# Kernel tuning notes

Measured on AMD Instinct MI355X. Metric: run time of the kernel, lower is better.

Reference implementation:

```python
import jax, jax.numpy as jnp
import numpy as np


def setup_inputs() -> dict:
    key = jax.random.key(0)
    ks = jax.random.split(key, 11)
    B, E, R, D = 2048, 20000, 500, 256
    inp = {
        "h": jax.random.uniform(ks[0], (B, E), dtype=jnp.float32),
        "t": jax.random.uniform(ks[1], (B, E), dtype=jnp.float32),
        "r": jax.random.uniform(ks[2], (B, R), dtype=jnp.float32),
        "W_er": jax.random.normal(ks[3], (D, E), dtype=jnp.float32) * 0.02,
        "W_ei": jax.random.normal(ks[4], (D, E), dtype=jnp.float32) * 0.02,
        "W_ej": jax.random.normal(ks[5], (D, E), dtype=jnp.float32) * 0.02,
        "W_ek": jax.random.normal(ks[6], (D, E), dtype=jnp.float32) * 0.02,
        "W_rr": jax.random.normal(ks[7], (D, R), dtype=jnp.float32) * 0.02,
        "W_ri": jax.random.normal(ks[8], (D, R), dtype=jnp.float32) * 0.02,
        "W_rj": jax.random.normal(ks[9], (D, R), dtype=jnp.float32) * 0.02,
        "W_rk": jax.random.normal(ks[10], (D, R), dtype=jnp.float32) * 0.02,
    }
    return inp


def reference(h, t, r, W_er, W_ei, W_ej, W_ek, W_rr, W_ri, W_rj, W_rk):
    # entity / relation projections (nn.Linear, no bias): x @ W^T -> [B, D]
    H_r, H_i, H_j, H_k = h @ W_er.T, h @ W_ei.T, h @ W_ej.T, h @ W_ek.T
    T_r, T_i, T_j, T_k = t @ W_er.T, t @ W_ei.T, t @ W_ej.T, t @ W_ek.T
    R_r, R_i, R_j, R_k = r @ W_rr.T, r @ W_ri.T, r @ W_rj.T, r @ W_rk.T

    # hypercomplex norm per row: sqrt(|R_r|^2 + |R_i|^2 + |R_j|^2 + |R_k|^2) -> [B,1]
    norm = jnp.sqrt(
        jnp.sum(R_r * R_r + R_i * R_i + R_j * R_j + R_k * R_k, axis=1, keepdims=True)
    )
    R_r, R_i, R_j, R_k = norm * R_r, norm * R_i, norm * R_j, norm * R_k

    # Hamilton product H (x) R
    Q_r = H_r * R_r - H_i * R_i - H_j * R_j - H_k * R_k
    Q_i = H_r * R_i + H_i * R_r + H_j * R_k - H_k * R_j
    Q_j = H_r * R_j - H_i * R_k + H_j * R_r + H_k * R_i
    Q_k = H_r * R_k + H_i * R_j - H_j * R_i + H_k * R_r

    # diag(Q @ T^T) == rowwise dot sum(Q*T, axis=1) -- O(B*d) form of the anti-pattern
    score = jnp.sum(Q_r * T_r + Q_i * T_i + Q_j * T_j + Q_k * T_k, axis=1, keepdims=True)
    return jax.nn.sigmoid(score)
```

## Files before the change

### kernel.cpp

```cpp
#include <hip/hip_runtime.h>


using bf16x8 = __attribute__((ext_vector_type(8))) short;
using f32x4  = __attribute__((ext_vector_type(4))) float;
using f32x16 = __attribute__((ext_vector_type(16))) float;

#define DEVINL static __device__ __forceinline__

DEVINL void split2(float x0, float x1, unsigned& h, unsigned& l) {
  unsigned u0 = __float_as_uint(x0), u1 = __float_as_uint(x1);
  unsigned h0 = u0 & 0xFFFF0000u, h1 = u1 & 0xFFFF0000u;
  h = (u0 >> 16) | h1;
  float r0 = x0 - __uint_as_float(h0);
  float r1 = x1 - __uint_as_float(h1);
  l = (__float_as_uint(r0) >> 16) | (__float_as_uint(r1) & 0xFFFF0000u);
}

DEVINL void gload16(const void* g, void* l) {
  __builtin_amdgcn_global_load_lds(
      (const __attribute__((address_space(1))) unsigned*)g,
      (__attribute__((address_space(3))) unsigned*)l, 16, 0, 0);
}

DEVINL void conv_body(const float* srow, int srcK, int kt, int rb,
                      char* dst, int ktiles, float ld[64][36], int t)
{
  {
    int r = t >> 2, kc = (t & 3) * 8;
    int k0 = kt * 32 + kc;
    const float* s = srow + (size_t)r * srcK;
    float4 v0, v1;
    if (k0 + 8 <= srcK) {
      v0 = *(const float4*)(s + k0);
      v1 = *(const float4*)(s + k0 + 4);
    } else {
      float x[8];
#pragma unroll
      for (int j = 0; j < 8; ++j) x[j] = (k0 + j < srcK) ? s[k0 + j] : 0.f;
      v0 = make_float4(x[0], x[1], x[2], x[3]);
      v1 = make_float4(x[4], x[5], x[6], x[7]);
    }
    *(float4*)&ld[r][kc]     = v0;
    *(float4*)&ld[r][kc + 4] = v1;
  }
  __syncthreads();
  {
    int g = t >> 7, s = (t >> 6) & 1, kh = (t >> 5) & 1, r31 = t & 31;
    int row = g * 32 + r31;
    int k = s * 16 + kh * 8;
    float x[8];
#pragma unroll
    for (int j = 0; j < 8; ++j) x[j] = ld[row][k + j];
    unsigned hh[4], llv[4];
    split2(x[0], x[1], hh[0], llv[0]);
    split2(x[2], x[3], hh[1], llv[1]);
    split2(x[4], x[5], hh[2], llv[2]);
    split2(x[6], x[7], hh[3], llv[3]);
    int tile_rt = rb >> 2;
    int gbase = (rb & 3) * 2;
    char* base = dst + ((size_t)tile_rt * ktiles + kt) * 32768
               + (gbase + g) * 2048 + s * 1024 + kh * 512 + r31 * 16;
    *(uint4*)base           = make_uint4(hh[0], hh[1], hh[2], hh[3]);
    *(uint4*)(base + 16384) = make_uint4(llv[0], llv[1], llv[2], llv[3]);
  }
}

__global__ void convert_img2(const float* __restrict__ src0,
                             const float* __restrict__ src1, int rows0,
                             int srcK, char* __restrict__ dst, int ktiles)
{
  __shared__ float ld[64][36];
  const int kt = blockIdx.x, rb = blockIdx.y, t = threadIdx.x;
  int row0 = rb * 64;
  const float* srow = (row0 < rows0) ? (src0 + (size_t)row0 * srcK)
                                     : (src1 + (size_t)(row0 - rows0) * srcK);
  conv_body(srow, srcK, kt, rb, dst, ktiles, ld, t);
}

__global__ void convert_q4(const float* __restrict__ p0, const float* __restrict__ p1,
                           const float* __restrict__ p2, const float* __restrict__ p3,
                           int rbPerQ, int srcK, char* __restrict__ dst,
                           size_t qStride, int ktiles)
{
  __shared__ float ld[64][36];
  const int kt = blockIdx.x, t = threadIdx.x;
  const int q = blockIdx.y / rbPerQ, rb = blockIdx.y % rbPerQ;
  const float* src = (q == 0) ? p0 : (q == 1) ? p1 : (q == 2) ? p2 : p3;
  conv_body(src + (size_t)(rb * 64) * srcK, srcK, kt, rb,
            dst + (size_t)q * qStride, ktiles, ld, t);
}

__global__ __launch_bounds__(512, 1) void gemm_img(
    const char* __restrict__ Aimg, const char* __restrict__ Bimg, int ktiles,
    float* __restrict__ C, int MT, int NT, int KS, int swz)
{
  __shared__ __align__(16) char smem[131072];
  const int bid = blockIdx.x;

  int mt, nt, ks;
  if (swz) {
    int x = bid & 7, w = bid >> 3;
    nt = w & 3;
    int g = x + (w >> 2) * 8;
    mt = g & 15; ks = g >> 4;
  } else {
    nt = bid % NT; int q = bid / NT; mt = q % MT; ks = q / MT;
  }

  const int kt0 = (ktiles * ks) / KS;
  const int kt1 = (ktiles * (ks + 1)) / KS;

  const char* Ab = Aimg + ((size_t)mt * ktiles + kt0) * 32768;
  const char* Bb = Bimg + ((size_t)nt * ktiles + kt0) * 32768;

  const int wid = threadIdx.x >> 6, lane = threadIdx.x & 63;
  const int wr = wid >> 2, wc = wid & 3;

  f32x16 acc[4][2];
#pragma unroll
  for (int mb = 0; mb < 4; ++mb)
#pragma unroll
    for (int nb = 0; nb < 2; ++nb)
#pragma unroll
      for (int e = 0; e < 16; ++e) acc[mb][nb][e] = 0.f;

  {
    const char* As = Ab + wid * 4096 + lane * 16;
    const char* Bs = Bb + wid * 4096 + lane * 16;
#pragma unroll
    for (int i = 0; i < 4; ++i) gload16(As + i * 1024, smem + wid * 4096 + i * 1024);
#pragma unroll
    for (int i = 0; i < 4; ++i) gload16(Bs + i * 1024, smem + 32768 + wid * 4096 + i * 1024);
  }
  asm volatile("s_waitcnt vmcnt(0)" ::: "memory");
  __builtin_amdgcn_s_barrier();

  for (int kt = kt0; kt < kt1; ++kt) {
    char* bufc = smem + (size_t)((kt - kt0) & 1) * 65536;
    char* bufn = smem + (size_t)(((kt - kt0) & 1) ^ 1) * 65536;
    const bool nx = (kt + 1 < kt1);

    if (nx) {
      const char* As = Ab + (size_t)(kt + 1 - kt0) * 32768 + wid * 4096 + lane * 16;
      const char* Bs = Bb + (size_t)(kt + 1 - kt0) * 32768 + wid * 4096 + lane * 16;
#pragma unroll
      for (int i = 0; i < 4; ++i) gload16(As + i * 1024, bufn + wid * 4096 + i * 1024);
#pragma unroll
      for (int i = 0; i < 4; ++i) gload16(Bs + i * 1024, bufn + 32768 + wid * 4096 + i * 1024);
    }

    bf16x8 bh[2][2], bl[2][2];
#pragma unroll
    for (int nb = 0; nb < 2; ++nb)
#pragma unroll
      for (int s = 0; s < 2; ++s) {
        const char* p = bufc + 32768 + (wc * 2 + nb) * 2048 + s * 1024 + lane * 16;
        bh[nb][s] = *(const bf16x8*)p;
        bl[nb][s] = *(const bf16x8*)(p + 16384);
      }

    __builtin_amdgcn_s_setprio(1);
#pragma unroll
    for (int mb = 0; mb < 4; ++mb) {
      const char* p = bufc + (wr * 4 + mb) * 2048 + lane * 16;
      bf16x8 ah0 = *(const bf16x8*)(p);
      bf16x8 al0 = *(const bf16x8*)(p + 16384);
      bf16x8 ah1 = *(const bf16x8*)(p + 1024);
      bf16x8 al1 = *(const bf16x8*)(p + 1024 + 16384);
#pragma unroll
      for (int nb = 0; nb < 2; ++nb) {
        f32x16* a = &acc[mb][nb];
        *a = __builtin_amdgcn_mfma_f32_32x32x16_bf16(ah0, bh[nb][0], *a, 0, 0, 0);
        *a = __builtin_amdgcn_mfma_f32_32x32x16_bf16(al0, bh[nb][0], *a, 0, 0, 0);
        *a = __builtin_amdgcn_mfma_f32_32x32x16_bf16(ah0, bl[nb][0], *a, 0, 0, 0);
        *a = __builtin_amdgcn_mfma_f32_32x32x16_bf16(ah1, bh[nb][1], *a, 0, 0, 0);
        *a = __builtin_amdgcn_mfma_f32_32x32x16_bf16(al1, bh[nb][1], *a, 0, 0, 0);
        *a = __builtin_amdgcn_mfma_f32_32x32x16_bf16(ah1, bl[nb][1], *a, 0, 0, 0);
      }
    }
    __builtin_amdgcn_s_setprio(0);

    asm volatile("s_waitcnt vmcnt(0)" ::: "memory");
    __builtin_amdgcn_s_barrier();
  }

  float* Cb = C + (size_t)ks * (size_t)(MT * 256) * 1024;
  const long rowbase = (long)mt * 256 + wr * 128 + 4 * (lane >> 5);
  const long colbase = (long)nt * 256 + wc * 64 + (lane & 31);
#pragma unroll
  for (int mb = 0; mb < 4; ++mb)
#pragma unroll
    for (int nb = 0; nb < 2; ++nb)
#pragma unroll
      for (int reg = 0; reg < 16; ++reg) {
        long row = rowbase + mb * 32 + (reg & 3) + 8 * (reg >> 2);
        long col = colbase + nb * 32;
        Cb[(size_t)row * 1024 + col] = acc[mb][nb][reg];
      }
}

__global__ __launch_bounds__(256) void epilogue_v4(
    const float* __restrict__ C1, const float* __restrict__ C2,
    float* __restrict__ out, int KS1, int KS2)
{
  const int w = threadIdx.x >> 6, lane = threadIdx.x & 63;
  const int b = blockIdx.x * 4 + w;
  const size_t SZ1 = 4096ull * 1024ull;
  const size_t SZ2 = 2048ull * 1024ull;
  const int c4 = lane * 4;

  float H[4][4], T[4][4], R[4][4];
#pragma unroll
  for (int q = 0; q < 4; ++q) {
    float4 hv = make_float4(0.f, 0.f, 0.f, 0.f);
    float4 tv = make_float4(0.f, 0.f, 0.f, 0.f);
    float4 rv = make_float4(0.f, 0.f, 0.f, 0.f);
    for (int ks = 0; ks < KS1; ++ks) {
      float4 a = *(const float4*)(C1 + ks * SZ1 + (size_t)b * 1024 + q * 256 + c4);
      float4 c = *(const float4*)(C1 + ks * SZ1 + (size_t)(b + 2048) * 1024 + q * 256 + c4);
      hv.x += a.x; hv.y += a.y; hv.z += a.z; hv.w += a.w;
      tv.x += c.x; tv.y += c.y; tv.z += c.z; tv.w += c.w;
    }
    for (int ks = 0; ks < KS2; ++ks) {
      float4 a = *(const float4*)(C2 + ks * SZ2 + (size_t)b * 1024 + q * 256 + c4);
      rv.x += a.x; rv.y += a.y; rv.z += a.z; rv.w += a.w;
    }
    H[q][0] = hv.x; H[q][1] = hv.y; H[q][2] = hv.z; H[q][3] = hv.w;
    T[q][0] = tv.x; T[q][1] = tv.y; T[q][2] = tv.z; T[q][3] = tv.w;
    R[q][0] = rv.x; R[q][1] = rv.y; R[q][2] = rv.z; R[q][3] = rv.w;
  }

  float ss = 0.f, nn = 0.f;
#pragma unroll
  for (int j = 0; j < 4; ++j) {
    float Hr = H[0][j], Hi = H[1][j], Hj = H[2][j], Hk = H[3][j];
    float Tr = T[0][j], Ti = T[1][j], Tj = T[2][j], Tk = T[3][j];
    float Rr = R[0][j], Ri = R[1][j], Rj = R[2][j], Rk = R[3][j];
    nn += Rr*Rr + Ri*Ri + Rj*Rj + Rk*Rk;
    float Qr = Hr*Rr - Hi*Ri - Hj*Rj - Hk*Rk;
    float Qi = Hr*Ri + Hi*Rr + Hj*Rk - Hk*Rj;
    float Qj = Hr*Rj - Hi*Rk + Hj*Rr + Hk*Ri;
    float Qk = Hr*Rk + Hi*Rj - Hj*Ri + Hk*Rr;
    ss += Qr*Tr + Qi*Ti + Qj*Tj + Qk*Tk;
  }
#pragma unroll
  for (int o = 32; o; o >>= 1) {
    ss += __shfl_xor(ss, o);
    nn += __shfl_xor(nn, o);
  }
  if (lane == 0) {
    float score = sqrtf(nn) * ss;
    out[b] = 1.f / (1.f + expf(-score));
  }
}

__global__ void convert_b16(const float* __restrict__ src, int srcK,
                            char* __restrict__ dst)
{
  const int tile = blockIdx.x;
  const int wrow = threadIdx.x;
  char* base = dst + (size_t)tile * 32768;
  const float* srow = src + (size_t)wrow * srcK;
#pragma unroll
  for (int kc8 = 0; kc8 < 4; ++kc8) {
    int k0 = tile * 32 + kc8 * 8;
    float x[8];
    if (k0 + 8 <= srcK) {
      float4 v0 = *(const float4*)(srow + k0);
      float4 v1 = *(const float4*)(srow + k0 + 4);
      x[0] = v0.x; x[1] = v0.y; x[2] = v0.z; x[3] = v0.w;
      x[4] = v1.x; x[5] = v1.y; x[6] = v1.z; x[7] = v1.w;
    } else {
#pragma unroll
      for (int j = 0; j < 8; ++j) x[j] = (k0 + j < srcK) ? srow[k0 + j] : 0.f;
    }
    unsigned hh[4], ll[4];
    split2(x[0], x[1], hh[0], ll[0]);
    split2(x[2], x[3], hh[1], ll[1]);
    split2(x[4], x[5], hh[2], ll[2]);
    split2(x[6], x[7], hh[3], ll[3]);
    int lchunk = (wrow & 15) + kc8 * 16;
    int n16 = wrow >> 4;
    *(uint4*)(base + (size_t)n16 * 1024 + lchunk * 16)         = make_uint4(hh[0], hh[1], hh[2], hh[3]);
    *(uint4*)(base + 16384 + (size_t)n16 * 1024 + lchunk * 16) = make_uint4(ll[0], ll[1], ll[2], ll[3]);
  }
}

__global__ void pad_r(const float* __restrict__ src, float* __restrict__ dst)
{
  int row = blockIdx.y;
  int k = threadIdx.x * 4;
  float4 v = make_float4(0.f, 0.f, 0.f, 0.f);
  if (k + 3 < 500) v = *(const float4*)(src + (size_t)row * 500 + k);
  *(float4*)(dst + (size_t)row * 512 + k) = v;
}

__global__ __launch_bounds__(512, 2) void gemm3p(
    const float* __restrict__ A0, const float* __restrict__ A1, int mtA0, long lda,
    const char* __restrict__ Bimg, int ktilesTot,
    float* __restrict__ C, long ldc, int MT, int NT, int KS, int swz)
{
  extern __shared__ char smemd[];
  const int tid = threadIdx.x;
  const int bid = blockIdx.x;

  int mt, nt, ks;
  if (swz) {
    int x = bid & 7, w = bid >> 3;
    nt = w & 3;
    int g = x + (w >> 2) * 8;
    mt = g & 15; ks = g >> 4;
  } else {
    nt = bid % NT; int q = bid / NT; mt = q % MT; ks = q / MT;
  }

  const int kt0 = (ktilesTot * ks) / KS;
  const int kt1 = (ktilesTot * (ks + 1)) / KS;

  const float* Ablk = (mt < mtA0) ? (A0 + (size_t)mt * 256 * lda)
                                  : (A1 + (size_t)(mt - mtA0) * 256 * lda);
  const char* Bt = Bimg + ((size_t)nt * ktilesTot + kt0) * 32768;

  const int wid = tid >> 6, lane = tid & 63;
  const int wr = wid >> 2, wc = wid & 3;
  const int l15 = lane & 15, lq = lane >> 4;

  const float* aSrc = Ablk + (size_t)(wid * 32 + (lane >> 3)) * lda
                      + (size_t)kt0 * 32 + 4 * (lane & 7);

  int awoff[4];
  {
    int kg = (lane & 7) >> 1, half = lane & 1;
#pragma unroll
    for (int i = 0; i < 4; ++i) {
      int m15 = (lane >> 3) + 8 * (i & 1);
      awoff[i] = (2 * wid + (i >> 1)) * 2048 + (((m15 ^ kg) + kg * 16) << 4) + half * 8;
    }
  }
  const int aroff = (((l15 ^ lq) + lq * 16) << 4);
  const int bbase = 32768 + (wc * 4) * 1024 + lane * 16;

  f32x4 acc[8][4];
#pragma unroll
  for (int m = 0; m < 8; ++m)
#pragma unroll
    for (int j = 0; j < 4; ++j)
#pragma unroll
      for (int e = 0; e < 4; ++e) acc[m][j][e] = 0.f;

  float4 aR[4];

#define ISSUE_A(KT)                                                            \
  {                                                                            \
    const float* p_ = aSrc + (size_t)((KT) - kt0) * 32;                        \
    _Pragma("unroll")                                                          \
    for (int i = 0; i < 4; ++i) aR[i] = *(const float4*)(p_ + (size_t)(8 * i) * lda); \
  }
#define ISSUE_B(DST, KT)                                                       \
  {                                                                            \
    const char* p_ = Bt + (size_t)((KT) - kt0) * 32768 + wid * 4096 + lane * 16; \
    _Pragma("unroll")                                                          \
    for (int i = 0; i < 4; ++i)                                                \
      gload16(p_ + i * 1024, (DST) + 32768 + wid * 4096 + i * 1024);           \
  }
#define WRITE_A(DST)                                                           \
  {                                                                            \
    _Pragma("unroll")                                                          \
    for (int i = 0; i < 4; ++i) {                                              \
      unsigned h0_, l0_, h1_, l1_;                                             \
      split2(aR[i].x, aR[i].y, h0_, l0_);                                      \
      split2(aR[i].z, aR[i].w, h1_, l1_);                                      \
      *(uint2*)((DST) + awoff[i])        = make_uint2(h0_, h1_);               \
      *(uint2*)((DST) + awoff[i] + 1024) = make_uint2(l0_, l1_);               \
    }                                                                          \
  }

  ISSUE_A(kt0);
  ISSUE_B(smemd, kt0);
  WRITE_A(smemd);
  asm volatile("s_waitcnt vmcnt(0)" ::: "memory");
  asm volatile("s_waitcnt lgkmcnt(0)" ::: "memory");
  __builtin_amdgcn_s_barrier();

  for (int kt = kt0; kt < kt1; ++kt) {
    char* bufc = smemd + (size_t)((kt - kt0) & 1) * 65536;
    char* bufn = smemd + (size_t)(((kt - kt0) & 1) ^ 1) * 65536;
    const bool nx = (kt + 1 < kt1);

    if (nx) { ISSUE_A(kt + 1); ISSUE_B(bufn, kt + 1); }

    bf16x8 bh[4], bl[4];
#pragma unroll
    for (int j = 0; j < 4; ++j) {
      bh[j] = *(const bf16x8*)(bufc + bbase + j * 1024);
      bl[j] = *(const bf16x8*)(bufc + bbase + j * 1024 + 16384);
    }

    __builtin_amdgcn_s_setprio(1);
#pragma unroll
    for (int m = 0; m < 4; ++m) {
      const char* ab = bufc + (wr * 8 + m) * 2048;
      bf16x8 ah = *(const bf16x8*)(ab + aroff);
      bf16x8 al = *(const bf16x8*)(ab + aroff + 1024);
#pragma unroll
      for (int j = 0; j < 4; ++j) {
        acc[m][j] = __builtin_amdgcn_mfma_f32_16x16x32_bf16(ah, bh[j], acc[m][j], 0, 0, 0);
        acc[m][j] = __builtin_amdgcn_mfma_f32_16x16x32_bf16(al, bh[j], acc[m][j], 0, 0, 0);
        acc[m][j] = __builtin_amdgcn_mfma_f32_16x16x32_bf16(ah, bl[j], acc[m][j], 0, 0, 0);
      }
    }
    __builtin_amdgcn_s_setprio(0);

    __builtin_amdgcn_sched_barrier(0);
    if (nx) WRITE_A(bufn);

    __builtin_amdgcn_s_setprio(1);
#pragma unroll
    for (int m = 4; m < 8; ++m) {
      const char* ab = bufc + (wr * 8 + m) * 2048;
      bf16x8 ah = *(const bf16x8*)(ab + aroff);
      bf16x8 al = *(const bf16x8*)(ab + aroff + 1024);
#pragma unroll
      for (int j = 0; j < 4; ++j) {
        acc[m][j] = __builtin_amdgcn_mfma_f32_16x16x32_bf16(ah, bh[j], acc[m][j], 0, 0, 0);
        acc[m][j] = __builtin_amdgcn_mfma_f32_16x16x32_bf16(al, bh[j], acc[m][j], 0, 0, 0);
        acc[m][j] = __builtin_amdgcn_mfma_f32_16x16x32_bf16(ah, bl[j], acc[m][j], 0, 0, 0);
      }
    }
    __builtin_amdgcn_s_setprio(0);

    asm volatile("s_waitcnt vmcnt(0)" ::: "memory");
    asm volatile("s_waitcnt lgkmcnt(0)" ::: "memory");
    __builtin_amdgcn_s_barrier();
  }
#undef ISSUE_A
#undef ISSUE_B
#undef WRITE_A

  float* Cb = C + (size_t)ks * (size_t)(MT * 256) * (size_t)ldc;
  const long rowbase = (long)mt * 256 + wr * 128 + lq * 4;
  const long colbase = (long)nt * 256 + wc * 64 + l15;
#pragma unroll
  for (int m = 0; m < 8; ++m)
#pragma unroll
    for (int j = 0; j < 4; ++j)
#pragma unroll
      for (int reg = 0; reg < 4; ++reg) {
        long row = rowbase + m * 16 + reg;
        long col = colbase + j * 16;
        Cb[(size_t)row * ldc + col] = acc[m][j][reg];
      }
}

__global__ void epilogue_kernel(const float* __restrict__ C1, const float* __restrict__ C2,
                                float* __restrict__ out, int KS1, int KS2)
{
  const int b = blockIdx.x;
  const int d = threadIdx.x;
  const size_t SZ1 = 4096ull * 1024ull;
  const size_t SZ2 = 2048ull * 1024ull;

  float Hq[4], Tq[4], Rq[4];
#pragma unroll
  for (int q = 0; q < 4; ++q) {
    float hv = 0.f, tv = 0.f, rv = 0.f;
    for (int ks = 0; ks < KS1; ++ks) {
      hv += C1[ks * SZ1 + (size_t)b * 1024 + q * 256 + d];
      tv += C1[ks * SZ1 + (size_t)(b + 2048) * 1024 + q * 256 + d];
    }
    for (int ks = 0; ks < KS2; ++ks)
      rv += C2[ks * SZ2 + (size_t)b * 1024 + q * 256 + d];
    Hq[q] = hv; Tq[q] = tv; Rq[q] = rv;
  }
  float nn = Rq[0]*Rq[0] + Rq[1]*Rq[1] + Rq[2]*Rq[2] + Rq[3]*Rq[3];
  float Qr = Hq[0]*Rq[0] - Hq[1]*Rq[1] - Hq[2]*Rq[2] - Hq[3]*Rq[3];
  float Qi = Hq[0]*Rq[1] + Hq[1]*Rq[0] + Hq[2]*Rq[3] - Hq[3]*Rq[2];
  float Qj = Hq[0]*Rq[2] - Hq[1]*Rq[3] + Hq[2]*Rq[0] + Hq[3]*Rq[1];
  float Qk = Hq[0]*Rq[3] + Hq[1]*Rq[2] - Hq[2]*Rq[1] + Hq[3]*Rq[0];
  float ss = Qr*Tq[0] + Qi*Tq[1] + Qj*Tq[2] + Qk*Tq[3];

#pragma unroll
  for (int o = 32; o; o >>= 1) {
    ss += __shfl_xor(ss, o);
    nn += __shfl_xor(nn, o);
  }
  __shared__ float red[8];
  int lane = d & 63, w = d >> 6;
  if (lane == 0) { red[w] = ss; red[4 + w] = nn; }
  __syncthreads();
  if (d == 0) {
    float S = red[0] + red[1] + red[2] + red[3];
    float N = red[4] + red[5] + red[6] + red[7];
    float score = sqrtf(N) * S;
    out[b] = 1.f / (1.f + expf(-score));
  }
}

extern "C" void kernel_launch(void* const* d_in, const int* in_sizes, int n_in,
                              void* d_out, int out_size, void* d_ws, size_t ws_size,
                              hipStream_t stream)
{
  const float* h = (const float*)d_in[0];
  const float* t = (const float*)d_in[1];
  const float* r = (const float*)d_in[2];
  const float* We[4] = {(const float*)d_in[3], (const float*)d_in[4],
                        (const float*)d_in[5], (const float*)d_in[6]};
  const float* Wr[4] = {(const float*)d_in[7], (const float*)d_in[8],
                        (const float*)d_in[9], (const float*)d_in[10]};
  float* out = (float*)d_out;
  char* ws = (char*)d_ws;

  const size_t offA  = 0;
  const size_t offB  = 327680000;
  const size_t offWr = offB + 81920000;
  const size_t offRi = offWr + 2097152;
  const size_t offC1 = offRi + 4194304;
  const size_t C1sz  = 4096ull * 1024ull * 4ull;
  const size_t C2sz  = 2048ull * 1024ull * 4ull;
  const size_t needImg = offC1 + 4 * C1sz;

  if (ws_size >= needImg) {
    float* C1 = (float*)(ws + offC1);
    float* C2 = (float*)(ws + offB);
    const int KS2 = 8;

    convert_img2<<<dim3(625, 64), 256, 0, stream>>>(h, t, 2048, 20000, ws + offA, 625);
    convert_q4<<<dim3(625, 16), 256, 0, stream>>>(
        We[0], We[1], We[2], We[3], 4, 20000, ws + offB, (size_t)625 * 32768, 625);
    convert_q4<<<dim3(16, 16), 256, 0, stream>>>(
        Wr[0], Wr[1], Wr[2], Wr[3], 4, 500, ws + offWr, (size_t)16 * 32768, 16);
    convert_img2<<<dim3(16, 32), 256, 0, stream>>>(r, r, 2048, 500, ws + offRi, 16);

    gemm_img<<<dim3(256), 512, 0, stream>>>(
        ws + offA, ws + offB, 625, C1, 16, 4, 4, 1);
    gemm_img<<<dim3(8 * 4 * KS2), 512, 0, stream>>>(
        ws + offRi, ws + offWr, 16, C2, 8, 4, KS2, 0);

    epilogue_v4<<<dim3(512), 256, 0, stream>>>(C1, C2, out, 4, KS2);
    return;
  }

  const size_t fB  = 0;
  const size_t fWr = 81920000;
  const size_t fR  = fWr + 2097152;
  const size_t fC1 = fR + 4194304;
  const int KS = (ws_size >= fC1 + 4 * C1sz + 8388608ull) ? 4 : 2;
  const size_t fC2 = fC1 + (size_t)KS * C1sz;

  float* rpad = (float*)(ws + fR);
  float* C1   = (float*)(ws + fC1);
  float* C2   = (float*)(ws + fC2);

  for (int q = 0; q < 4; ++q) {
    convert_b16<<<dim3(625), 256, 0, stream>>>(We[q], 20000, ws + fB + (size_t)q * 625 * 32768);
    convert_b16<<<dim3(16), 256, 0, stream>>>(Wr[q], 500, ws + fWr + (size_t)q * 16 * 32768);
  }
  pad_r<<<dim3(1, 2048), 128, 0, stream>>>(r, rpad);

  gemm3p<<<dim3(16 * 4 * KS), 512, 131072, stream>>>(
      h, t, 8, 20000L, (const char*)(ws + fB), 625,
      C1, 1024L, 16, 4, KS, KS == 4 ? 1 : 0);
  gemm3p<<<dim3(32), 512, 131072, stream>>>(
      rpad, rpad, 8, 512L, (const char*)(ws + fWr), 16,
      C2, 1024L, 8, 4, 1, 0);

  epilogue_kernel<<<dim3(2048), 256, 0, stream>>>(C1, C2, out, KS, 1);
}
```

Baseline: 594.5 us.

## Replace double-buffered GEMM loop with four-slot half-tile ring pipeline

Splits each K tile into two half-steps and keeps a four-slot shared-memory ring, issuing loads three stages ahead. The old loop waited on all outstanding loads with vmcnt(0) every step; the new loop uses partial vmcnt waits so global-to-LDS transfers overlap with MFMA work. The cost is a more intricate prologue and epilogue sequence, with a risk of stalls or wrong results if the vmcnt counts or slot reuse are off. The MFMA count per tile and the LDS footprint of 128KB stay the same.

Measured after the change: 574.7 us. -3.3%, faster.

```diff
diff --git a/kernel.cpp b/kernel.cpp
--- a/kernel.cpp
+++ b/kernel.cpp
@@ -90,7 +90,7 @@
             dst + (size_t)q * qStride, ktiles, ld, t);
 }
 
-__global__ __launch_bounds__(512, 1) void gemm_img(
+__global__ __launch_bounds__(512, 1) void gemm_ring(
     const char* __restrict__ Aimg, const char* __restrict__ Bimg, int ktiles,
     float* __restrict__ C, int MT, int NT, int KS, int swz)
 {
@@ -109,6 +109,7 @@
 
   const int kt0 = (ktiles * ks) / KS;
   const int kt1 = (ktiles * (ks + 1)) / KS;
+  const int nsteps = 2 * (kt1 - kt0);
 
   const char* Ab = Aimg + ((size_t)mt * ktiles + kt0) * 32768;
   const char* Bb = Bimg + ((size_t)nt * ktiles + kt0) * 32768;
@@ -124,65 +125,77 @@
 #pragma unroll
       for (int e = 0; e < 16; ++e) acc[mb][nb][e] = 0.f;
 
-  {
-    const char* As = Ab + wid * 4096 + lane * 16;
-    const char* Bs = Bb + wid * 4096 + lane * 16;
-#pragma unroll
-    for (int i = 0; i < 4; ++i) gload16(As + i * 1024, smem + wid * 4096 + i * 1024);
-#pragma unroll
-    for (int i = 0; i < 4; ++i) gload16(Bs + i * 1024, smem + 32768 + wid * 4096 + i * 1024);
-  }
+#define STAGE(S)                                                               \
+  {                                                                            \
+    char* slot_ = smem + ((S) & 3) * 32768;                                    \
+    const char* At_ = Ab + (size_t)((S) >> 1) * 32768;                         \
+    const char* Bt_ = Bb + (size_t)((S) >> 1) * 32768;                         \
+    const int ko_ = ((S) & 1) * 1024;                                          \
+    _Pragma("unroll")                                                          \
+    for (int i = 0; i < 2; ++i) {                                              \
+      int p_ = 2 * wid + i;                                                    \
+      int src_ = (p_ >> 3) * 16384 + (p_ & 7) * 2048 + ko_ + lane * 16;        \
+      gload16(At_ + src_, slot_ + p_ * 1024);                                  \
+      gload16(Bt_ + src_, slot_ + 16384 + p_ * 1024);                          \
+    }                                                                          \
+  }
+#define COMPUTE(S)                                                             \
+  {                                                                            \
+    const char* slot_ = smem + ((S) & 3) * 32768;                              \
+    bf16x8 a_[4][2], b_[2][2];                                                 \
+    _Pragma("unroll")                                                          \
+    for (int mb = 0; mb < 4; ++mb)                                             \
+      _Pragma("unroll")                                                        \
+      for (int pl = 0; pl < 2; ++pl)                                           \
+        a_[mb][pl] = *(const bf16x8*)(slot_ + (pl * 8 + wr * 4 + mb) * 1024    \
+                                      + lane * 16);                            \
+    _Pragma("unroll")                                                          \
+    for (int nb = 0; nb < 2; ++nb)                                             \
+      _Pragma("unroll")                                                        \
+      for (int pl = 0; pl < 2; ++pl)                                           \
+        b_[nb][pl] = *(const bf16x8*)(slot_ + 16384                            \
+                                      + (pl * 8 + wc * 2 + nb) * 1024         \
+                                      + lane * 16);                            \
+    __builtin_amdgcn_s_setprio(1);                                             \
+    _Pragma("unroll")                                                          \
+    for (int mb = 0; mb < 4; ++mb)                                             \
+      _Pragma("unroll")                                                        \
+      for (int nb = 0; nb < 2; ++nb) {                                         \
+        f32x16* c_ = &acc[mb][nb];                                             \
+        *c_ = __builtin_amdgcn_mfma_f32_32x32x16_bf16(a_[mb][0], b_[nb][0], *c_, 0, 0, 0); \
+        *c_ = __builtin_amdgcn_mfma_f32_32x32x16_bf16(a_[mb][1], b_[nb][0], *c_, 0, 0, 0); \
+        *c_ = __builtin_amdgcn_mfma_f32_32x32x16_bf16(a_[mb][0], b_[nb][1], *c_, 0, 0, 0); \
+      }                                                                        \
+    __builtin_amdgcn_s_setprio(0);                                             \
+  }
+
+  STAGE(0); STAGE(1); STAGE(2);
+  asm volatile("s_waitcnt vmcnt(8)" ::: "memory");
+  __builtin_amdgcn_sched_barrier(0);
+  __builtin_amdgcn_s_barrier();
+
+  int s = 0;
+  for (; s + 3 < nsteps; ++s) {
+    STAGE(s + 3);
+    __builtin_amdgcn_sched_barrier(0);
+    COMPUTE(s);
+    __builtin_amdgcn_sched_barrier(0);
+    asm volatile("s_waitcnt vmcnt(8)" ::: "memory");
+    __builtin_amdgcn_s_barrier();
+  }
+  COMPUTE(s);
+  __builtin_amdgcn_sched_barrier(0);
+  asm volatile("s_waitcnt vmcnt(4)" ::: "memory");
+  __builtin_amdgcn_s_barrier();
+  ++s;
+  COMPUTE(s);
+  __builtin_amdgcn_sched_barrier(0);
   asm volatile("s_waitcnt vmcnt(0)" ::: "memory");
   __builtin_amdgcn_s_barrier();
-
-  for (int kt = kt0; kt < kt1; ++kt) {
-    char* bufc = smem + (size_t)((kt - kt0) & 1) * 65536;
-    char* bufn = smem + (size_t)(((kt - kt0) & 1) ^ 1) * 65536;
-    const bool nx = (kt + 1 < kt1);
-
-    if (nx) {
-      const char* As = Ab + (size_t)(kt + 1 - kt0) * 32768 + wid * 4096 + lane * 16;
-      const char* Bs = Bb + (size_t)(kt + 1 - kt0) * 32768 + wid * 4096 + lane * 16;
-#pragma unroll
-      for (int i = 0; i < 4; ++i) gload16(As + i * 1024, bufn + wid * 4096 + i * 1024);
-#pragma unroll
-      for (int i = 0; i < 4; ++i) gload16(Bs + i * 1024, bufn + 32768 + wid * 4096 + i * 1024);
-    }
-
-    bf16x8 bh[2][2], bl[2][2];
-#pragma unroll
-    for (int nb = 0; nb < 2; ++nb)
-#pragma unroll
-      for (int s = 0; s < 2; ++s) {
-        const char* p = bufc + 32768 + (wc * 2 + nb) * 2048 + s * 1024 + lane * 16;
-        bh[nb][s] = *(const bf16x8*)p;
-        bl[nb][s] = *(const bf16x8*)(p + 16384);
-      }
-
-    __builtin_amdgcn_s_setprio(1);
-#pragma unroll
-    for (int mb = 0; mb < 4; ++mb) {
-      const char* p = bufc + (wr * 4 + mb) * 2048 + lane * 16;
-      bf16x8 ah0 = *(const bf16x8*)(p);
-      bf16x8 al0 = *(const bf16x8*)(p + 16384);
-      bf16x8 ah1 = *(const bf16x8*)(p + 1024);
-      bf16x8 al1 = *(const bf16x8*)(p + 1024 + 16384);
-#pragma unroll
-      for (int nb = 0; nb < 2; ++nb) {
-        f32x16* a = &acc[mb][nb];
-        *a = __builtin_amdgcn_mfma_f32_32x32x16_bf16(ah0, bh[nb][0], *a, 0, 0, 0);
-        *a = __builtin_amdgcn_mfma_f32_32x32x16_bf16(al0, bh[nb][0], *a, 0, 0, 0);
-        *a = __builtin_amdgcn_mfma_f32_32x32x16_bf16(ah0, bl[nb][0], *a, 0, 0, 0);
-        *a = __builtin_amdgcn_mfma_f32_32x32x16_bf16(ah1, bh[nb][1], *a, 0, 0, 0);
-        *a = __builtin_amdgcn_mfma_f32_32x32x16_bf16(al1, bh[nb][1], *a, 0, 0, 0);
-        *a = __builtin_amdgcn_mfma_f32_32x32x16_bf16(ah1, bl[nb][1], *a, 0, 0, 0);
-      }
-    }
-    __builtin_amdgcn_s_setprio(0);
-
-    asm volatile("s_waitcnt vmcnt(0)" ::: "memory");
-    __builtin_amdgcn_s_barrier();
-  }
+  ++s;
+  COMPUTE(s);
+#undef STAGE
+#undef COMPUTE
 
   float* Cb = C + (size_t)ks * (size_t)(MT * 256) * 1024;
   const long rowbase = (long)mt * 256 + wr * 128 + 4 * (lane >> 5);
@@ -531,9 +544,9 @@
         Wr[0], Wr[1], Wr[2], Wr[3], 4, 500, ws + offWr, (size_t)16 * 32768, 16);
     convert_img2<<<dim3(16, 32), 256, 0, stream>>>(r, r, 2048, 500, ws + offRi, 16);
 
-    gemm_img<<<dim3(256), 512, 0, stream>>>(
+    gemm_ring<<<dim3(256), 512, 0, stream>>>(
         ws + offA, ws + offB, 625, C1, 16, 4, 4, 1);
-    gemm_img<<<dim3(8 * 4 * KS2), 512, 0, stream>>>(
+    gemm_ring<<<dim3(8 * 4 * KS2), 512, 0, stream>>>(
         ws + offRi, ws + offWr, 16, C2, 8, 4, KS2, 0);
 
     epilogue_v4<<<dim3(512), 256, 0, stream>>>(C1, C2, out, 4, KS2);
```
